# Optimization experiments

Hardware: AMD Instinct MI355X
Metric: run time of the kernel (lower is better)

## Reference

```python
import jax, jax.numpy as jnp
import numpy as np

N = 1000000
SH_COEFFS = 16  # (sh_degree+1)^2 with sh_degree=3
H = 256
W = 256
K_RENDER = 1000  # module renders min(1000, N) front-most-by-descending-depth splats


def setup_inputs():
    key = jax.random.key(0)
    k = jax.random.split(key, 5)
    positions = jax.random.normal(k[0], (N, 3), jnp.float32) * 0.1
    scales = jnp.ones((N, 3), jnp.float32) * 0.01
    rotations = jax.random.normal(k[1], (N, 4), jnp.float32)
    colors = jax.random.normal(k[2], (N, 3), jnp.float32)
    opacity = jnp.ones((N, 1), jnp.float32) * 0.1
    colors_sh = jax.random.normal(k[3], (N, SH_COEFFS, 3), jnp.float32) * 0.001
    # realistic pinhole camera: fx=fy=500, cx=cy=128, translation z=2 so depths>0
    camera_matrix = jnp.array([[500.0, 0.0, 128.0, 0.0],
                               [0.0, 500.0, 128.0, 0.0],
                               [0.0, 0.0, 1.0, 2.0]], jnp.float32)
    camera_position = jax.random.normal(k[4], (3,), jnp.float32) * 0.1
    return {"positions": positions, "scales": scales, "rotations": rotations,
            "colors": colors, "opacity": opacity, "colors_sh": colors_sh,
            "camera_matrix": camera_matrix, "camera_position": camera_position,
            "image_height": H, "image_width": W}


def _covariance(scales, rotations):
    # Sigma = R S S^T R^T, quaternion -> rotation matrix
    q = rotations / jnp.linalg.norm(rotations, axis=-1, keepdims=True)
    w, x, y, z = q[:, 0], q[:, 1], q[:, 2], q[:, 3]
    R = jnp.stack([
        jnp.stack([1 - 2 * (y * y + z * z), 2 * (x * y - w * z), 2 * (x * z + w * y)], -1),
        jnp.stack([2 * (x * y + w * z), 1 - 2 * (x * x + z * z), 2 * (y * z - w * x)], -1),
        jnp.stack([2 * (x * z - w * y), 2 * (y * z + w * x), 1 - 2 * (x * x + y * y)], -1)], -2)  # [N,3,3]
    s2 = jnp.clip(scales, 1e-7, None) ** 2
    return jnp.einsum('nij,nj,nkj->nik', R, s2, R)


def _sh_bases(d):
    x, y, z = d[:, 0], d[:, 1], d[:, 2]
    return jnp.stack([
        jnp.full_like(x, 0.28209479177387814),
        -0.48860251190291987 * y, 0.48860251190291987 * z, -0.48860251190291987 * x,
        1.0925484305920792 * x * y, -1.0925484305920792 * y * z,
        0.31539156525252005 * (2 * z * z - x * x - y * y),
        -1.0925484305920792 * x * z, 0.5462742152960396 * (x * x - y * y)], -1)  # [N,9]


def _forward(positions, scales, rotations, colors, opacity, colors_sh,
             camera_matrix, camera_position, image_height, image_width):
    cov3d = _covariance(jnp.exp(scales), rotations)  # [N,3,3]
    # perspective projection
    pos_h = jnp.concatenate([positions, jnp.ones((positions.shape[0], 1), positions.dtype)], -1)
    proj = pos_h @ camera_matrix.T  # [N,3]
    depths = proj[:, 2]
    pos2d = proj[:, :2] / (depths[:, None] + 1e-7)
    fx, fy = camera_matrix[0, 0], camera_matrix[1, 1]
    zero = jnp.zeros_like(depths)
    J = jnp.stack([
        jnp.stack([fx / depths, zero, -fx * pos2d[:, 0] / depths], -1),
        jnp.stack([zero, fy / depths, -fy * pos2d[:, 1] / depths], -1)], -2)  # [N,2,3]
    cov2d = jnp.einsum('nij,njk,nlk->nil', J, cov3d, J)  # [N,2,2]
    # view-dependent color via SH (only first 9 bases, as in the torch loop)
    vd = positions - camera_position[None]
    vd = vd / jnp.linalg.norm(vd, axis=-1, keepdims=True)
    sh = _sh_bases(vd)
    col = jax.nn.sigmoid(colors + jnp.einsum('nkc,nk->nc', colors_sh[:, :sh.shape[-1]], sh))
    op = jax.nn.sigmoid(opacity[:, 0])
    # depth sort descending, keep first K_RENDER (matches min(1000, N) loop)
    order = jnp.argsort(-depths)[:K_RENDER]
    mu_s, cov_s, col_s, op_s = pos2d[order], cov2d[order], col[order], op[order]
    ys = jnp.arange(image_height, dtype=jnp.float32)
    xs = jnp.arange(image_width, dtype=jnp.float32)
    yy, xx = jnp.meshgrid(ys, xs, indexing='ij')
    px = xx.reshape(-1)
    py = yy.reshape(-1)  # [P]
    P = image_height * image_width

    def step(carry, g):
        rendered, acc = carry
        mu, cv, c, o = g
        # 2x2 inverse of (cov + 1e-6 I), closed form
        a = cv[0, 0] + 1e-6
        b = cv[0, 1]
        cc = cv[1, 0]
        d = cv[1, 1] + 1e-6
        det = a * d - b * cc
        dx = px - mu[0]
        dy = py - mu[1]
        qv = (d * dx * dx - (b + cc) * dx * dy + a * dy * dy) / det
        alpha = o * jnp.exp(-0.5 * qv)           # [P]
        contrib = (1.0 - acc) * alpha            # front-to-back compositing
        rendered = rendered + contrib[:, None] * c
        acc = acc + contrib
        return (rendered, acc), None

    init = (jnp.zeros((P, 3), jnp.float32), jnp.zeros((P,), jnp.float32))
    (rendered, _), _ = jax.lax.scan(step, init, (mu_s, cov_s, col_s, op_s))
    return rendered.reshape(image_height, image_width, 3)


def reference(positions, scales, rotations, colors, opacity, colors_sh,
              camera_matrix, camera_position, image_height, image_width):
    return _forward(positions, scales, rotations, colors, opacity, colors_sh,
                    camera_matrix, camera_position, image_height, image_width)
```

## Files before the change

kernel.cpp:

```cpp
#include <hip/hip_runtime.h>
#include <stdint.h>

typedef uint32_t u32;
typedef uint64_t u64;

#define KREN 1000
#define CAND0_CAP 16384
#define CAND_CAP 4096
#define GSTRIDE 12
#define SEGN 16
#define P0_BLK 512
#define P1_BLK 512
#define P2_BLK 32
#define P3_BLK 1024

__device__ __forceinline__ u32 fkey(float f) {
  u32 b = __float_as_uint(f);
  return (b & 0x80000000u) ? ~b : (b | 0x80000000u);
}

__device__ __forceinline__ void pick_scan256(const u32* __restrict__ hist, u32 K,
                                             u32* lds, int* bin_out, u32* Krem_out) {
  int tid = threadIdx.x;
  u32 hv[16];
  u32 s = 0;
#pragma unroll
  for (int k = 0; k < 16; ++k) { hv[k] = hist[tid * 16 + k]; s += hv[k]; }
  lds[tid] = s;
  __syncthreads();
  for (int d = 1; d < 256; d <<= 1) {
    u32 v = lds[tid] + ((tid + d < 256) ? lds[tid + d] : 0u);
    __syncthreads();
    lds[tid] = v;
    __syncthreads();
  }
  u32 inc = lds[tid];
  u32 above = (tid < 255) ? lds[tid + 1] : 0u;
  if (above < K && inc >= K) {
    u32 cum = above;
    for (int k = 15; k >= 0; --k) {
      cum += hv[k];
      if (cum >= K) {
        lds[256] = (u32)(tid * 16 + k);
        lds[257] = K - (cum - hv[k]);
        break;
      }
    }
  }
  __syncthreads();
  *bin_out = (int)lds[256];
  *Krem_out = lds[257];
  __syncthreads();
}

__global__ __launch_bounds__(256) void k_p0(const float* __restrict__ pos,
                                            const float* __restrict__ cam,
                                            u32* __restrict__ keys,
                                            u32* __restrict__ hist1, int N) {
  __shared__ u32 hl[4096];
  int tid = threadIdx.x;
  int lane = tid & 63;
  for (int i = tid; i < 4096; i += 256) hl[i] = 0;
  __syncthreads();
  float c8 = cam[8], c9 = cam[9], c10 = cam[10], c11 = cam[11];
  for (int i = blockIdx.x * 256 + tid; i < N; i += P0_BLK * 256) {
    float x = pos[3 * i], y = pos[3 * i + 1], z = pos[3 * i + 2];
    u32 mk = fkey(c8 * x + c9 * y + c10 * z + c11);
    keys[i] = mk;
    u32 bin = mk >> 20;
    u64 todo = __ballot(true);
    while (todo) {
      int leader = __ffsll((unsigned long long)todo) - 1;
      u32 lbin = __shfl(bin, leader, 64);
      u64 same = __ballot(bin == lbin);
      if (lane == leader) atomicAdd(&hl[lbin], (u32)__popcll(same & todo));
      todo &= ~same;
    }
  }
  __syncthreads();
  for (int i = tid; i < 4096; i += 256) {
    u32 v = hl[i];
    if (v) atomicAdd(&hist1[i], v);
  }
}

__global__ __launch_bounds__(256) void k_p1(const u32* __restrict__ keys,
                                            const u32* __restrict__ hist1,
                                            u32* __restrict__ hist2,
                                            u64* __restrict__ cand0,
                                            u32* __restrict__ state, int N) {
  __shared__ u32 hl[4096];
  __shared__ u32 sl[258];
  int tid = threadIdx.x;
  int lane = tid & 63;
  int bin1; u32 K1;
  pick_scan256(hist1, (u32)KREN, sl, &bin1, &K1);
  if (tid == 0) { state[4] = K1; state[5] = (u32)bin1; }
  u32 pref = (u32)bin1;
  for (int i = tid; i < 4096; i += 256) hl[i] = 0;
  __syncthreads();
  for (int i = blockIdx.x * 256 + tid; i < N; i += P1_BLK * 256) {
    u32 k = keys[i];
    bool m = (k >> 20) == pref;
    if (m) atomicAdd(&hl[(k >> 8) & 4095u], 1u);
    u64 bm = __ballot(m);
    if (bm) {
      u32 base;
      int leader = __ffsll((unsigned long long)bm) - 1;
      if (lane == leader) base = atomicAdd(&state[1], (u32)__popcll(bm));
      base = __shfl(base, leader, 64);
      if (m) {
        u32 p = base + (u32)__popcll(bm & ((1ull << lane) - 1ull));
        if (p < CAND0_CAP) cand0[p] = (((u64)(~k)) << 32) | (u32)i;
      }
    }
  }
  __syncthreads();
  for (int i = tid; i < 4096; i += 256) {
    u32 v = hl[i];
    if (v) atomicAdd(&hist2[i], v);
  }
}

__global__ __launch_bounds__(256) void k_p2(const u64* __restrict__ cand0,
                                            const u32* __restrict__ hist2,
                                            u64* __restrict__ cand,
                                            u32* __restrict__ state) {
  __shared__ u32 sl[258];
  int tid = threadIdx.x;
  int lane = tid & 63;
  u32 K1 = state[4];
  u32 pref = state[5];
  int bin2; u32 K2;
  pick_scan256(hist2, K1, sl, &bin2, &K2);
  u32 Thi = ~((pref << 20) | (((u32)bin2) << 8));
  int M1 = (int)state[1];
  if (M1 > CAND0_CAP) M1 = CAND0_CAP;
  for (int i = blockIdx.x * 256 + tid; i < M1; i += P2_BLK * 256) {
    u64 e = cand0[i];
    bool m = (u32)(e >> 32) <= Thi;
    u64 bm = __ballot(m);
    if (bm) {
      u32 base;
      int leader = __ffsll((unsigned long long)bm) - 1;
      if (lane == leader) base = atomicAdd(&state[0], (u32)__popcll(bm));
      base = __shfl(base, leader, 64);
      if (m) {
        u32 p = base + (u32)__popcll(bm & ((1ull << lane) - 1ull));
        if (p < CAND_CAP) cand[p] = e;
      }
    }
  }
}

__global__ __launch_bounds__(256) void k_p3(
    const u64* __restrict__ cand, const u32* __restrict__ state,
    const float* __restrict__ pos, const float* __restrict__ scales,
    const float* __restrict__ rot, const float* __restrict__ colors,
    const float* __restrict__ opac, const float* __restrict__ csh,
    const float* __restrict__ cam, const float* __restrict__ campos,
    float* __restrict__ gauss, int shstride) {
  __shared__ u64 sc[CAND_CAP];
  int tid = threadIdx.x, bid = blockIdx.x;
  int lane = tid & 63;
  int M = (int)state[0];
  if (M > CAND_CAP) M = CAND_CAP;
  if (bid * 4 >= M) return;
  for (int i = tid; i < M; i += 256) sc[i] = cand[i];
  __syncthreads();
  int c = bid * 4 + (tid >> 6);
  if (c >= M) return;
  u64 mine = sc[c];
  int cnt = 0;
  int JJ = (M + 63) >> 6;
  for (int jj = 0; jj < JJ; ++jj) {
    int j = lane + (jj << 6);
    if (j < M && sc[j] < mine) ++cnt;
  }
#pragma unroll
  for (int d = 32; d; d >>= 1) cnt += __shfl_xor(cnt, d, 64);
  int r = cnt;
  if (r >= KREN || lane != 0) return;
  int g = (int)(u32)(mine & 0xffffffffu);
  float x = pos[3 * g], y = pos[3 * g + 1], z = pos[3 * g + 2];
  float c0 = cam[0], c1 = cam[1], c2 = cam[2], c3 = cam[3];
  float c4 = cam[4], c5 = cam[5], c6 = cam[6], c7 = cam[7];
  float c8 = cam[8], c9 = cam[9], c10 = cam[10], c11 = cam[11];
  float dep = c8 * x + c9 * y + c10 * z + c11;
  float invd = 1.0f / (dep + 1e-7f);
  float p2x = (c0 * x + c1 * y + c2 * z + c3) * invd;
  float p2y = (c4 * x + c5 * y + c6 * z + c7) * invd;
  float qw = rot[4 * g], qx = rot[4 * g + 1], qy = rot[4 * g + 2], qz = rot[4 * g + 3];
  float qn = rsqrtf(qw * qw + qx * qx + qy * qy + qz * qz);
  qw *= qn; qx *= qn; qy *= qn; qz *= qn;
  float r00 = 1.f - 2.f * (qy * qy + qz * qz), r01 = 2.f * (qx * qy - qw * qz), r02 = 2.f * (qx * qz + qw * qy);
  float r10 = 2.f * (qx * qy + qw * qz), r11 = 1.f - 2.f * (qx * qx + qz * qz), r12 = 2.f * (qy * qz - qw * qx);
  float r20 = 2.f * (qx * qz - qw * qy), r21 = 2.f * (qy * qz + qw * qx), r22 = 1.f - 2.f * (qx * qx + qy * qy);
  float e0 = fmaxf(expf(scales[3 * g]), 1e-7f);
  float e1 = fmaxf(expf(scales[3 * g + 1]), 1e-7f);
  float e2 = fmaxf(expf(scales[3 * g + 2]), 1e-7f);
  float v0 = e0 * e0, v1 = e1 * e1, v2 = e2 * e2;
  float C00 = r00 * r00 * v0 + r01 * r01 * v1 + r02 * r02 * v2;
  float C01 = r00 * r10 * v0 + r01 * r11 * v1 + r02 * r12 * v2;
  float C02 = r00 * r20 * v0 + r01 * r21 * v1 + r02 * r22 * v2;
  float C11 = r10 * r10 * v0 + r11 * r11 * v1 + r12 * r12 * v2;
  float C12 = r10 * r20 * v0 + r11 * r21 * v1 + r12 * r22 * v2;
  float C22 = r20 * r20 * v0 + r21 * r21 * v1 + r22 * r22 * v2;
  float fx = c0, fy = c5;
  float jd = 1.0f / dep;
  float j0 = fx * jd, j2 = -fx * p2x * jd, j4 = fy * jd, j5 = -fy * p2y * jd;
  float u0x = j0 * C00 + j2 * C02;
  float u0y = j0 * C01 + j2 * C12;
  float u0z = j0 * C02 + j2 * C22;
  float u1y = j4 * C11 + j5 * C12;
  float u1z = j4 * C12 + j5 * C22;
  float a = u0x * j0 + u0z * j2 + 1e-6f;
  float b = u0y * j4 + u0z * j5;
  float d2 = u1y * j4 + u1z * j5 + 1e-6f;
  float det = a * d2 - b * b;
  float idet = 1.0f / det;
  const float L = 1.4426950408889634f;
  float Aq = -0.5f * L * d2 * idet;
  float Bq = L * b * idet;
  float Cq = -0.5f * L * a * idet;
  float vx = x - campos[0], vy = y - campos[1], vz = z - campos[2];
  float vn = rsqrtf(vx * vx + vy * vy + vz * vz);
  vx *= vn; vy *= vn; vz *= vn;
  float sh[9];
  sh[0] = 0.28209479177387814f;
  sh[1] = -0.48860251190291987f * vy;
  sh[2] = 0.48860251190291987f * vz;
  sh[3] = -0.48860251190291987f * vx;
  sh[4] = 1.0925484305920792f * vx * vy;
  sh[5] = -1.0925484305920792f * vy * vz;
  sh[6] = 0.31539156525252005f * (2.f * vz * vz - vx * vx - vy * vy);
  sh[7] = -1.0925484305920792f * vx * vz;
  sh[8] = 0.5462742152960396f * (vx * vx - vy * vy);
  float col[3];
  for (int c2 = 0; c2 < 3; ++c2) {
    float accv = colors[3 * g + c2];
    for (int k2 = 0; k2 < 9; ++k2) accv += sh[k2] * csh[(size_t)g * shstride + 3 * k2 + c2];
    col[c2] = 1.0f / (1.0f + __expf(-accv));
  }
  float op = 1.0f / (1.0f + __expf(-opac[g]));
  float* G = gauss + r * GSTRIDE;
  G[0] = p2x; G[1] = p2y; G[2] = Aq; G[3] = Bq; G[4] = Cq;
  G[5] = op;  G[6] = col[0]; G[7] = col[1]; G[8] = col[2];
  G[9] = 0.f; G[10] = 0.f; G[11] = 0.f;
}

__global__ __launch_bounds__(1024) void k_p4(const float* __restrict__ gauss,
                                             float* __restrict__ out) {
  __shared__ u64 smem[8192];
  int tid = threadIdx.x, bid = blockIdx.x;
  float* gs = (float*)smem;
  float4* g4s = (float4*)smem;
  const float4* g4 = (const float4*)gauss;
  for (int i = tid; i < 3000; i += 1024) g4s[i] = g4[i];
  __syncthreads();
  int grp = tid & 63;
  int seg = tid >> 6;
  float pxf = (float)(grp * 4);
  float pyf = (float)bid;
  float cr0 = 0.f, cr1 = 0.f, cr2 = 0.f, cr3 = 0.f;
  float cg0 = 0.f, cg1 = 0.f, cg2 = 0.f, cg3 = 0.f;
  float cb0 = 0.f, cb1 = 0.f, cb2 = 0.f, cb3 = 0.f;
  float ac0 = 0.f, ac1 = 0.f, ac2 = 0.f, ac3 = 0.f;
  int gbeg = (seg * KREN) / SEGN, gend = ((seg + 1) * KREN) / SEGN;
  for (int k = gbeg; k < gend; ++k) {
    const float4* Gp = (const float4*)(gs + k * GSTRIDE);
    float4 g0 = Gp[0];
    float4 g1 = Gp[1];
    float g2x = gs[k * GSTRIDE + 8];
    float A = g0.z, B = g0.w, C = g1.x, op = g1.y;
    float dx = pxf - g0.x, dy = pyf - g0.y;
    float q0 = (A * dx + B * dy) * dx + C * dy * dy;
    float u = 2.f * A * dx + B * dy;
    float q1 = q0 + u + A;
    float q2 = q0 + 2.f * u + 4.f * A;
    float q3 = q0 + 3.f * u + 9.f * A;
    float e0 = op * exp2f(q0), e1 = op * exp2f(q1);
    float e2 = op * exp2f(q2), e3 = op * exp2f(q3);
    float w0 = (1.f - ac0) * e0, w1 = (1.f - ac1) * e1;
    float w2 = (1.f - ac2) * e2, w3 = (1.f - ac3) * e3;
    cr0 += w0 * g1.z; cg0 += w0 * g1.w; cb0 += w0 * g2x; ac0 += w0;
    cr1 += w1 * g1.z; cg1 += w1 * g1.w; cb1 += w1 * g2x; ac1 += w1;
    cr2 += w2 * g1.z; cg2 += w2 * g1.w; cb2 += w2 * g2x; ac2 += w2;
    cr3 += w3 * g1.z; cg3 += w3 * g1.w; cb3 += w3 * g2x; ac3 += w3;
  }
  __syncthreads();
  float4* comb = (float4*)smem;
  int base = seg * 256 + grp * 4;
  comb[base + 0] = make_float4(cr0, cg0, cb0, 1.f - ac0);
  comb[base + 1] = make_float4(cr1, cg1, cb1, 1.f - ac1);
  comb[base + 2] = make_float4(cr2, cg2, cb2, 1.f - ac2);
  comb[base + 3] = make_float4(cr3, cg3, cb3, 1.f - ac3);
  __syncthreads();
  if (tid < 256) {
    int px = tid;
    float R = 0.f, Gc = 0.f, Bc = 0.f, T = 1.f;
#pragma unroll
    for (int s2 = 0; s2 < SEGN; ++s2) {
      float4 cv = comb[s2 * 256 + px];
      R += T * cv.x; Gc += T * cv.y; Bc += T * cv.z;
      T *= cv.w;
    }
    int p = bid * 256 + px;
    out[3 * p + 0] = R;
    out[3 * p + 1] = Gc;
    out[3 * p + 2] = Bc;
  }
}

extern "C" void kernel_launch(void* const* d_in, const int* in_sizes, int n_in,
                              void* d_out, int out_size, void* d_ws, size_t ws_size,
                              hipStream_t stream) {
  const float* positions = (const float*)d_in[0];
  const float* scales    = (const float*)d_in[1];
  const float* rotations = (const float*)d_in[2];
  const float* colors    = (const float*)d_in[3];
  const float* opacity   = (const float*)d_in[4];
  const float* colors_sh = (const float*)d_in[5];
  const float* cam       = (const float*)d_in[6];
  const float* campos    = (const float*)d_in[7];
  int N = in_sizes[0] / 3;
  int shstride = in_sizes[5] / N;

  char* ws = (char*)d_ws;
  u32* keys    = (u32*)ws;
  u64* cand0   = (u64*)(ws + 4194304);
  u64* cand    = (u64*)(ws + 4325376);
  float* gauss = (float*)(ws + 4358144);
  char* zr     = ws + 4407296;
  u32* hist1   = (u32*)zr;
  u32* hist2   = (u32*)(zr + 16384);
  u32* state   = (u32*)(zr + 32768);
  float* out   = (float*)d_out;

  hipMemsetAsync(zr, 0, 33280, stream);
  k_p0<<<P0_BLK, 256, 0, stream>>>(positions, cam, keys, hist1, N);
  k_p1<<<P1_BLK, 256, 0, stream>>>(keys, hist1, hist2, cand0, state, N);
  k_p2<<<P2_BLK, 256, 0, stream>>>(cand0, hist2, cand, state);
  k_p3<<<P3_BLK, 256, 0, stream>>>(cand, state, positions, scales, rotations,
                                   colors, opacity, colors_sh, cam, campos,
                                   gauss, shstride);
  k_p4<<<256, 1024, 0, stream>>>(gauss, out);
}
```

Baseline: 378.1 us.

## Drop second radix pass, vectorize key passes, add early-exit per-pixel compositing

Replaces the two-level histogram selection with a single pass that collects every key at or above the 1000th-ranked top-level bin, and removes the k_p2 filter kernel. The rank step now reads candidates straight from global memory instead of staging them in LDS. k_p0 and k_p1 read positions and keys as float4/uint4. The renderer switches from a 16-segment split with a merge step to one thread per pixel that stages the first 256 gaussians in LDS and leaves the loop once the whole wavefront is saturated. The risks are more rank work when many keys share the cutoff bin, O(M^2) global reads, and fewer threads per pixel in the renderer. Early exit also drops contributions once transmittance falls below 1e-7, and the float4 reads assume N is a multiple of 4.

```diff
diff --git a/kernel.cpp b/kernel.cpp
--- a/kernel.cpp
+++ b/kernel.cpp
@@ -6,21 +6,18 @@
 
 #define KREN 1000
 #define CAND0_CAP 16384
-#define CAND_CAP 4096
 #define GSTRIDE 12
-#define SEGN 16
+#define STAGE_N 256
 #define P0_BLK 512
 #define P1_BLK 512
-#define P2_BLK 32
-#define P3_BLK 1024
 
 __device__ __forceinline__ u32 fkey(float f) {
   u32 b = __float_as_uint(f);
   return (b & 0x80000000u) ? ~b : (b | 0x80000000u);
 }
 
-__device__ __forceinline__ void pick_scan256(const u32* __restrict__ hist, u32 K,
-                                             u32* lds, int* bin_out, u32* Krem_out) {
+__device__ __forceinline__ int pick_scan256(const u32* __restrict__ hist, u32 K,
+                                            u32* lds) {
   int tid = threadIdx.x;
   u32 hv[16];
   u32 s = 0;
@@ -40,17 +37,13 @@
     u32 cum = above;
     for (int k = 15; k >= 0; --k) {
       cum += hv[k];
-      if (cum >= K) {
-        lds[256] = (u32)(tid * 16 + k);
-        lds[257] = K - (cum - hv[k]);
-        break;
-      }
+      if (cum >= K) { lds[256] = (u32)(tid * 16 + k); break; }
     }
   }
   __syncthreads();
-  *bin_out = (int)lds[256];
-  *Krem_out = lds[257];
-  __syncthreads();
+  int bin = (int)lds[256];
+  __syncthreads();
+  return bin;
 }
 
 __global__ __launch_bounds__(256) void k_p0(const float* __restrict__ pos,
@@ -63,18 +56,28 @@
   for (int i = tid; i < 4096; i += 256) hl[i] = 0;
   __syncthreads();
   float c8 = cam[8], c9 = cam[9], c10 = cam[10], c11 = cam[11];
-  for (int i = blockIdx.x * 256 + tid; i < N; i += P0_BLK * 256) {
-    float x = pos[3 * i], y = pos[3 * i + 1], z = pos[3 * i + 2];
-    u32 mk = fkey(c8 * x + c9 * y + c10 * z + c11);
-    keys[i] = mk;
-    u32 bin = mk >> 20;
-    u64 todo = __ballot(true);
-    while (todo) {
-      int leader = __ffsll((unsigned long long)todo) - 1;
-      u32 lbin = __shfl(bin, leader, 64);
-      u64 same = __ballot(bin == lbin);
-      if (lane == leader) atomicAdd(&hl[lbin], (u32)__popcll(same & todo));
-      todo &= ~same;
+  const float4* p4 = (const float4*)pos;
+  uint4* k4 = (uint4*)keys;
+  int NG = N >> 2;
+  for (int g = blockIdx.x * 256 + tid; g < NG; g += P0_BLK * 256) {
+    float4 v0 = p4[3 * g], v1 = p4[3 * g + 1], v2 = p4[3 * g + 2];
+    u32 b0 = fkey(c8 * v0.x + c9 * v0.y + c10 * v0.z + c11);
+    u32 b1 = fkey(c8 * v0.w + c9 * v1.x + c10 * v1.y + c11);
+    u32 b2 = fkey(c8 * v1.z + c9 * v1.w + c10 * v2.x + c11);
+    u32 b3 = fkey(c8 * v2.y + c9 * v2.z + c10 * v2.w + c11);
+    k4[g] = make_uint4(b0, b1, b2, b3);
+    u32 bins[4] = {b0 >> 20, b1 >> 20, b2 >> 20, b3 >> 20};
+#pragma unroll
+    for (int s = 0; s < 4; ++s) {
+      u32 bin = bins[s];
+      u64 todo = __ballot(true);
+      while (todo) {
+        int leader = __ffsll((unsigned long long)todo) - 1;
+        u32 lbin = __shfl(bin, leader, 64);
+        u64 same = __ballot(bin == lbin);
+        if (lane == leader) atomicAdd(&hl[lbin], (u32)__popcll(same & todo));
+        todo &= ~same;
+      }
     }
   }
   __syncthreads();
@@ -86,97 +89,52 @@
 
 __global__ __launch_bounds__(256) void k_p1(const u32* __restrict__ keys,
                                             const u32* __restrict__ hist1,
-                                            u32* __restrict__ hist2,
                                             u64* __restrict__ cand0,
                                             u32* __restrict__ state, int N) {
-  __shared__ u32 hl[4096];
   __shared__ u32 sl[258];
   int tid = threadIdx.x;
   int lane = tid & 63;
-  int bin1; u32 K1;
-  pick_scan256(hist1, (u32)KREN, sl, &bin1, &K1);
-  if (tid == 0) { state[4] = K1; state[5] = (u32)bin1; }
-  u32 pref = (u32)bin1;
-  for (int i = tid; i < 4096; i += 256) hl[i] = 0;
-  __syncthreads();
-  for (int i = blockIdx.x * 256 + tid; i < N; i += P1_BLK * 256) {
-    u32 k = keys[i];
-    bool m = (k >> 20) == pref;
-    if (m) atomicAdd(&hl[(k >> 8) & 4095u], 1u);
-    u64 bm = __ballot(m);
-    if (bm) {
-      u32 base;
-      int leader = __ffsll((unsigned long long)bm) - 1;
-      if (lane == leader) base = atomicAdd(&state[1], (u32)__popcll(bm));
-      base = __shfl(base, leader, 64);
-      if (m) {
-        u32 p = base + (u32)__popcll(bm & ((1ull << lane) - 1ull));
-        if (p < CAND0_CAP) cand0[p] = (((u64)(~k)) << 32) | (u32)i;
+  int bin1 = pick_scan256(hist1, (u32)KREN, sl);
+  u32 T = ((u32)bin1) << 20;
+  const uint4* k4 = (const uint4*)keys;
+  int NG = N >> 2;
+  for (int g = blockIdx.x * 256 + tid; g < NG; g += P1_BLK * 256) {
+    uint4 kv = k4[g];
+    u32 ka[4] = {kv.x, kv.y, kv.z, kv.w};
+#pragma unroll
+    for (int s = 0; s < 4; ++s) {
+      bool m = ka[s] >= T;
+      u64 bm = __ballot(m);
+      if (bm) {
+        u32 base;
+        int leader = __ffsll((unsigned long long)bm) - 1;
+        if (lane == leader) base = atomicAdd(&state[1], (u32)__popcll(bm));
+        base = __shfl(base, leader, 64);
+        if (m) {
+          u32 p = base + (u32)__popcll(bm & ((1ull << lane) - 1ull));
+          if (p < CAND0_CAP) cand0[p] = (((u64)(~ka[s])) << 32) | (u32)(4 * g + s);
+        }
       }
     }
   }
-  __syncthreads();
-  for (int i = tid; i < 4096; i += 256) {
-    u32 v = hl[i];
-    if (v) atomicAdd(&hist2[i], v);
-  }
-}
-
-__global__ __launch_bounds__(256) void k_p2(const u64* __restrict__ cand0,
-                                            const u32* __restrict__ hist2,
-                                            u64* __restrict__ cand,
-                                            u32* __restrict__ state) {
-  __shared__ u32 sl[258];
-  int tid = threadIdx.x;
-  int lane = tid & 63;
-  u32 K1 = state[4];
-  u32 pref = state[5];
-  int bin2; u32 K2;
-  pick_scan256(hist2, K1, sl, &bin2, &K2);
-  u32 Thi = ~((pref << 20) | (((u32)bin2) << 8));
-  int M1 = (int)state[1];
-  if (M1 > CAND0_CAP) M1 = CAND0_CAP;
-  for (int i = blockIdx.x * 256 + tid; i < M1; i += P2_BLK * 256) {
-    u64 e = cand0[i];
-    bool m = (u32)(e >> 32) <= Thi;
-    u64 bm = __ballot(m);
-    if (bm) {
-      u32 base;
-      int leader = __ffsll((unsigned long long)bm) - 1;
-      if (lane == leader) base = atomicAdd(&state[0], (u32)__popcll(bm));
-      base = __shfl(base, leader, 64);
-      if (m) {
-        u32 p = base + (u32)__popcll(bm & ((1ull << lane) - 1ull));
-        if (p < CAND_CAP) cand[p] = e;
-      }
-    }
-  }
 }
 
 __global__ __launch_bounds__(256) void k_p3(
-    const u64* __restrict__ cand, const u32* __restrict__ state,
+    const u64* __restrict__ cand0, const u32* __restrict__ state,
     const float* __restrict__ pos, const float* __restrict__ scales,
     const float* __restrict__ rot, const float* __restrict__ colors,
     const float* __restrict__ opac, const float* __restrict__ csh,
     const float* __restrict__ cam, const float* __restrict__ campos,
     float* __restrict__ gauss, int shstride) {
-  __shared__ u64 sc[CAND_CAP];
   int tid = threadIdx.x, bid = blockIdx.x;
   int lane = tid & 63;
-  int M = (int)state[0];
-  if (M > CAND_CAP) M = CAND_CAP;
-  if (bid * 4 >= M) return;
-  for (int i = tid; i < M; i += 256) sc[i] = cand[i];
-  __syncthreads();
+  int M = (int)state[1];
+  if (M > CAND0_CAP) M = CAND0_CAP;
   int c = bid * 4 + (tid >> 6);
   if (c >= M) return;
-  u64 mine = sc[c];
+  u64 mine = cand0[c];
   int cnt = 0;
-  int JJ = (M + 63) >> 6;
-  for (int jj = 0; jj < JJ; ++jj) {
-    int j = lane + (jj << 6);
-    if (j < M && sc[j] < mine) ++cnt;
-  }
+  for (int j = lane; j < M; j += 64) cnt += (cand0[j] < mine) ? 1 : 0;
 #pragma unroll
   for (int d = 32; d; d >>= 1) cnt += __shfl_xor(cnt, d, 64);
   int r = cnt;
@@ -249,67 +207,48 @@
   G[9] = 0.f; G[10] = 0.f; G[11] = 0.f;
 }
 
-__global__ __launch_bounds__(1024) void k_p4(const float* __restrict__ gauss,
-                                             float* __restrict__ out) {
-  __shared__ u64 smem[8192];
+__global__ __launch_bounds__(256) void k_p4(const float* __restrict__ gauss,
+                                            float* __restrict__ out) {
+  __shared__ float gs[STAGE_N * GSTRIDE];
   int tid = threadIdx.x, bid = blockIdx.x;
-  float* gs = (float*)smem;
-  float4* g4s = (float4*)smem;
   const float4* g4 = (const float4*)gauss;
-  for (int i = tid; i < 3000; i += 1024) g4s[i] = g4[i];
-  __syncthreads();
-  int grp = tid & 63;
-  int seg = tid >> 6;
-  float pxf = (float)(grp * 4);
-  float pyf = (float)bid;
-  float cr0 = 0.f, cr1 = 0.f, cr2 = 0.f, cr3 = 0.f;
-  float cg0 = 0.f, cg1 = 0.f, cg2 = 0.f, cg3 = 0.f;
-  float cb0 = 0.f, cb1 = 0.f, cb2 = 0.f, cb3 = 0.f;
-  float ac0 = 0.f, ac1 = 0.f, ac2 = 0.f, ac3 = 0.f;
-  int gbeg = (seg * KREN) / SEGN, gend = ((seg + 1) * KREN) / SEGN;
-  for (int k = gbeg; k < gend; ++k) {
+  float4* g4s = (float4*)gs;
+  for (int i = tid; i < STAGE_N * 3; i += 256) g4s[i] = g4[i];
+  __syncthreads();
+  int p = bid * 256 + tid;
+  float px = (float)(p & 255);
+  float py = (float)(p >> 8);
+  float cr = 0.f, cg = 0.f, cb = 0.f, acc = 0.f;
+  int k = 0;
+  for (; k < STAGE_N; ++k) {
     const float4* Gp = (const float4*)(gs + k * GSTRIDE);
     float4 g0 = Gp[0];
     float4 g1 = Gp[1];
     float g2x = gs[k * GSTRIDE + 8];
-    float A = g0.z, B = g0.w, C = g1.x, op = g1.y;
-    float dx = pxf - g0.x, dy = pyf - g0.y;
-    float q0 = (A * dx + B * dy) * dx + C * dy * dy;
-    float u = 2.f * A * dx + B * dy;
-    float q1 = q0 + u + A;
-    float q2 = q0 + 2.f * u + 4.f * A;
-    float q3 = q0 + 3.f * u + 9.f * A;
-    float e0 = op * exp2f(q0), e1 = op * exp2f(q1);
-    float e2 = op * exp2f(q2), e3 = op * exp2f(q3);
-    float w0 = (1.f - ac0) * e0, w1 = (1.f - ac1) * e1;
-    float w2 = (1.f - ac2) * e2, w3 = (1.f - ac3) * e3;
-    cr0 += w0 * g1.z; cg0 += w0 * g1.w; cb0 += w0 * g2x; ac0 += w0;
-    cr1 += w1 * g1.z; cg1 += w1 * g1.w; cb1 += w1 * g2x; ac1 += w1;
-    cr2 += w2 * g1.z; cg2 += w2 * g1.w; cb2 += w2 * g2x; ac2 += w2;
-    cr3 += w3 * g1.z; cg3 += w3 * g1.w; cb3 += w3 * g2x; ac3 += w3;
-  }
-  __syncthreads();
-  float4* comb = (float4*)smem;
-  int base = seg * 256 + grp * 4;
-  comb[base + 0] = make_float4(cr0, cg0, cb0, 1.f - ac0);
-  comb[base + 1] = make_float4(cr1, cg1, cb1, 1.f - ac1);
-  comb[base + 2] = make_float4(cr2, cg2, cb2, 1.f - ac2);
-  comb[base + 3] = make_float4(cr3, cg3, cb3, 1.f - ac3);
-  __syncthreads();
-  if (tid < 256) {
-    int px = tid;
-    float R = 0.f, Gc = 0.f, Bc = 0.f, T = 1.f;
-#pragma unroll
-    for (int s2 = 0; s2 < SEGN; ++s2) {
-      float4 cv = comb[s2 * 256 + px];
-      R += T * cv.x; Gc += T * cv.y; Bc += T * cv.z;
-      T *= cv.w;
-    }
-    int p = bid * 256 + px;
-    out[3 * p + 0] = R;
-    out[3 * p + 1] = Gc;
-    out[3 * p + 2] = Bc;
-  }
+    float dx = px - g0.x, dy = py - g0.y;
+    float sE = g0.z * dx * dx + g0.w * dx * dy + g1.x * dy * dy;
+    float alpha = g1.y * exp2f(sE);
+    float w = (1.0f - acc) * alpha;
+    cr += w * g1.z; cg += w * g1.w; cb += w * g2x;
+    acc += w;
+    if (__all((1.0f - acc) < 1e-7f)) { k = KREN; break; }
+  }
+  for (; k < KREN; ++k) {
+    const float4* Gp = (const float4*)(gauss + k * GSTRIDE);
+    float4 g0 = Gp[0];
+    float4 g1 = Gp[1];
+    float g2x = gauss[k * GSTRIDE + 8];
+    float dx = px - g0.x, dy = py - g0.y;
+    float sE = g0.z * dx * dx + g0.w * dx * dy + g1.x * dy * dy;
+    float alpha = g1.y * exp2f(sE);
+    float w = (1.0f - acc) * alpha;
+    cr += w * g1.z; cg += w * g1.w; cb += w * g2x;
+    acc += w;
+    if (__all((1.0f - acc) < 1e-7f)) break;
+  }
+  out[3 * p + 0] = cr;
+  out[3 * p + 1] = cg;
+  out[3 * p + 2] = cb;
 }
 
 extern "C" void kernel_launch(void* const* d_in, const int* in_sizes, int n_in,
@@ -329,20 +268,17 @@
   char* ws = (char*)d_ws;
   u32* keys    = (u32*)ws;
   u64* cand0   = (u64*)(ws + 4194304);
-  u64* cand    = (u64*)(ws + 4325376);
-  float* gauss = (float*)(ws + 4358144);
-  char* zr     = ws + 4407296;
+  float* gauss = (float*)(ws + 4325376);
+  char* zr     = ws + 4374528;
   u32* hist1   = (u32*)zr;
-  u32* hist2   = (u32*)(zr + 16384);
-  u32* state   = (u32*)(zr + 32768);
+  u32* state   = (u32*)(zr + 16384);
   float* out   = (float*)d_out;
 
-  hipMemsetAsync(zr, 0, 33280, stream);
+  hipMemsetAsync(zr, 0, 16640, stream);
   k_p0<<<P0_BLK, 256, 0, stream>>>(positions, cam, keys, hist1, N);
-  k_p1<<<P1_BLK, 256, 0, stream>>>(keys, hist1, hist2, cand0, state, N);
-  k_p2<<<P2_BLK, 256, 0, stream>>>(cand0, hist2, cand, state);
-  k_p3<<<P3_BLK, 256, 0, stream>>>(cand, state, positions, scales, rotations,
-                                   colors, opacity, colors_sh, cam, campos,
-                                   gauss, shstride);
-  k_p4<<<256, 1024, 0, stream>>>(gauss, out);
-}
+  k_p1<<<P1_BLK, 256, 0, stream>>>(keys, hist1, cand0, state, N);
+  k_p3<<<CAND0_CAP / 4, 256, 0, stream>>>(cand0, state, positions, scales, rotations,
+                                          colors, opacity, colors_sh, cam, campos,
+                                          gauss, shstride);
+  k_p4<<<256, 256, 0, stream>>>(gauss, out);
+}
```

After: 363.2 us. -3.9%, faster.
